# Performance work log

Hardware: AMD Instinct MI355X
Metric: run time of the kernel (lower is better)

The kernel has to match this reference:

```python
import jax, jax.numpy as jnp
import numpy as np

C = 192; H = 8; DH = C // H; FF = 384; SET = 36; NSET = 2048; N = NSET * SET
NBLK = 4; NLYR = 8
EPS = 1e-5
SCALE = np.float32(1.0 / np.sqrt(DH))


def _ln(x, w, b):
    m = jnp.mean(x, -1, keepdims=True)
    v = jnp.mean((x - m) ** 2, -1, keepdims=True)
    return (x - m) * jax.lax.rsqrt(v + EPS) * w + b


def _set_attn(src, pos, inds, mask, l, in_w, in_b, ow, ob, l1w, l1b, l2w, l2b, n1w, n1b, n2w, n2b):
    # gather voxel features into sets: [NSET, SET, C]
    feat = src[inds]
    q = feat + pos[inds]  # query == key == feat + pos_embed; value == feat
    qp = (q @ in_w[l, :C].T + in_b[l, :C]).reshape(NSET, SET, H, DH)
    kp = (q @ in_w[l, C:2 * C].T + in_b[l, C:2 * C]).reshape(NSET, SET, H, DH)
    vp = (feat @ in_w[l, 2 * C:].T + in_b[l, 2 * C:]).reshape(NSET, SET, H, DH)
    scores = jnp.einsum('sqhd,skhd->shqk', qp, kp) * SCALE
    scores = jnp.where(mask[:, None, None, :], jnp.float32(-1e9), scores)
    attn = jax.nn.softmax(scores, axis=-1)
    o = jnp.einsum('shqk,skhd->sqhd', attn, vp).reshape(NSET, SET, C)
    o = o @ ow[l].T + ob[l]
    # onnx_export scatter-back: placeholder[flatten_inds] = src2 (inds are a permutation)
    src2 = jnp.zeros_like(src).at[inds.reshape(-1)].set(o.reshape(-1, C))
    x = _ln(src + src2, n1w[l], n1b[l])
    ff = jax.nn.relu(x @ l1w[l].T + l1b[l]) @ l2w[l].T + l2b[l]
    return _ln(x + ff, n2w[l], n2b[l])


def _forward(feats, pos_embed, inds0, inds1, mask0, mask1, in_w, in_b, ow, ob,
             l1w, l1b, l2w, l2b, n1w, n1b, n2w, n2b, enw, enb, bnw, bnb):
    out = feats
    res = out
    for blk in range(NBLK):
        inds_t = inds0 if blk % 2 == 0 else inds1
        mask_t = mask0 if blk % 2 == 0 else mask1
        for s in range(2):
            l = 2 * blk + s
            ident = out
            x = _set_attn(out, pos_embed[blk, s], inds_t[s], mask_t[s], l,
                          in_w, in_b, ow, ob, l1w, l1b, l2w, l2b, n1w, n1b, n2w, n2b)
            out = _ln(x + ident, enw[l], enb[l])
        out = _ln(res + out, bnw[blk], bnb[blk])
        res = out
    return out


def setup_inputs() -> dict:
    key = jax.random.key(0)
    ks = jax.random.split(key, 16)
    s = jnp.float32(0.02)

    def perm(k):
        return jax.random.permutation(k, N).reshape(NSET, SET).astype(jnp.int32)

    inds0 = jnp.stack([perm(ks[1]), perm(ks[2])])
    inds1 = jnp.stack([perm(ks[3]), perm(ks[4])])
    mask0 = jnp.zeros((2, NSET, SET), dtype=bool)
    mask1 = jnp.zeros((2, NSET, SET), dtype=bool)
    return {
        'pillar_features': jax.random.normal(ks[0], (N, C), jnp.float32),
        'set_voxel_inds_tensor_shift_0': inds0,
        'set_voxel_inds_tensor_shift_1': inds1,
        'set_voxel_masks_tensor_shift_0': mask0,
        'set_voxel_masks_tensor_shift_1': mask1,
        'pos_embed_tensor': jax.random.normal(ks[5], (NBLK, 2, N, C), jnp.float32) * s,
        'in_proj_w': jax.random.normal(ks[6], (NLYR, 3 * C, C), jnp.float32) * s,
        'in_proj_b': jnp.zeros((NLYR, 3 * C), jnp.float32),
        'out_proj_w': jax.random.normal(ks[7], (NLYR, C, C), jnp.float32) * s,
        'out_proj_b': jnp.zeros((NLYR, C), jnp.float32),
        'lin1_w': jax.random.normal(ks[8], (NLYR, FF, C), jnp.float32) * s,
        'lin1_b': jnp.zeros((NLYR, FF), jnp.float32),
        'lin2_w': jax.random.normal(ks[9], (NLYR, C, FF), jnp.float32) * s,
        'lin2_b': jnp.zeros((NLYR, C), jnp.float32),
        'norm1_w': jnp.ones((NLYR, C), jnp.float32),
        'norm1_b': jnp.zeros((NLYR, C), jnp.float32),
        'norm2_w': jnp.ones((NLYR, C), jnp.float32),
        'norm2_b': jnp.zeros((NLYR, C), jnp.float32),
        'enc_norm_w': jnp.ones((NLYR, C), jnp.float32),
        'enc_norm_b': jnp.zeros((NLYR, C), jnp.float32),
        'blk_norm_w': jnp.ones((NBLK, C), jnp.float32),
        'blk_norm_b': jnp.zeros((NBLK, C), jnp.float32),
    }


def reference(pillar_features, set_voxel_inds_tensor_shift_0, set_voxel_inds_tensor_shift_1,
              set_voxel_masks_tensor_shift_0, set_voxel_masks_tensor_shift_1, pos_embed_tensor,
              in_proj_w, in_proj_b, out_proj_w, out_proj_b, lin1_w, lin1_b, lin2_w, lin2_b,
              norm1_w, norm1_b, norm2_w, norm2_b, enc_norm_w, enc_norm_b, blk_norm_w, blk_norm_b):
    return _forward(pillar_features, pos_embed_tensor,
                    set_voxel_inds_tensor_shift_0, set_voxel_inds_tensor_shift_1,
                    set_voxel_masks_tensor_shift_0, set_voxel_masks_tensor_shift_1,
                    in_proj_w, in_proj_b, out_proj_w, out_proj_b,
                    lin1_w, lin1_b, lin2_w, lin2_b,
                    norm1_w, norm1_b, norm2_w, norm2_b,
                    enc_norm_w, enc_norm_b, blk_norm_w, blk_norm_b)
```

## Files before the change

kernel.cpp:

```cpp
#include <hip/hip_runtime.h>
#include <stdint.h>


#define CC 192
#define FFD 384
#define NSETS 2048
#define SETSZ 36
#define NVOX (NSETS * SETSZ)
#define NCELEM ((size_t)NVOX * CC)
#define EPSV 1e-5f
#define SCALEV 0.2041241452319315f

typedef __bf16 bf16x8 __attribute__((ext_vector_type(8)));
typedef float f32x4 __attribute__((ext_vector_type(4)));

__device__ __forceinline__ float bflo(unsigned int u) {
  union { unsigned int i; float f; } v; v.i = u << 16; return v.f;
}
__device__ __forceinline__ float bfhi(unsigned int u) {
  union { unsigned int i; float f; } v; v.i = u & 0xffff0000u; return v.f;
}
__device__ __forceinline__ float bf2f(unsigned short s) {
  union { unsigned int i; float f; } v; v.i = ((unsigned int)s) << 16; return v.f;
}
__device__ __forceinline__ unsigned short f2bf(float f) {
  union { float f; unsigned int i; } v; v.f = f;
  return (unsigned short)((v.i + 0x7fffu + ((v.i >> 16) & 1u)) >> 16);
}
__device__ __forceinline__ unsigned int pack2(float a, float b) {
  return (unsigned int)f2bf(a) | ((unsigned int)f2bf(b) << 16);
}
__device__ __forceinline__ float wsum64(float v) {
#pragma unroll
  for (int off = 32; off > 0; off >>= 1) v += __shfl_xor(v, off, 64);
  return v;
}

__global__ __launch_bounds__(256) void cvt_xp(const float* __restrict__ pf,
                                              const float* __restrict__ pos,
                                              unsigned short* __restrict__ R,
                                              unsigned short* __restrict__ XP) {
  const size_t i = (size_t)blockIdx.x * 256 + threadIdx.x;
  const float4 a = ((const float4*)pf)[2 * i];
  const float4 b = ((const float4*)pf)[2 * i + 1];
  const float4 p = ((const float4*)pos)[2 * i];
  const float4 q = ((const float4*)pos)[2 * i + 1];
  uint4 r, x;
  r.x = pack2(a.x, a.y); r.y = pack2(a.z, a.w);
  r.z = pack2(b.x, b.y); r.w = pack2(b.z, b.w);
  x.x = pack2(a.x + p.x, a.y + p.y); x.y = pack2(a.z + p.z, a.w + p.w);
  x.z = pack2(b.x + q.x, b.y + q.y); x.w = pack2(b.z + q.z, b.w + q.w);
  ((uint4*)R)[i] = r;
  ((uint4*)XP)[i] = x;
}

__global__ __launch_bounds__(256) void cvt_wfrag(const float* __restrict__ src,
                                                 unsigned short* __restrict__ dst,
                                                 int N, int K, int total) {
  const int t = blockIdx.x * 256 + threadIdx.x;
  if (t >= total) return;
  const int lane = t & 63;
  const int f = t >> 6;
  const int nks = K >> 5;
  const int ks = f % nks;
  const int rem = f / nks;
  const int nnt = N >> 4;
  const int nt = rem % nnt;
  const int l = rem / nnt;
  const int row = nt * 16 + (lane & 15);
  const int k0 = ks * 32 + (lane >> 4) * 8;
  const float* s = src + ((size_t)l * N + row) * K + k0;
  const float4 a = *(const float4*)s;
  const float4 b = *(const float4*)(s + 4);
  uint4 o;
  o.x = pack2(a.x, a.y); o.y = pack2(a.z, a.w);
  o.z = pack2(b.x, b.y); o.w = pack2(b.z, b.w);
  *(uint4*)(dst + (size_t)t * 8) = o;
}

__global__ __launch_bounds__(256, 2) void qkvattn_kernel(
    const unsigned short* __restrict__ XP, const unsigned short* __restrict__ Xv,
    const int* __restrict__ inds, const unsigned short* __restrict__ Wf,
    const float* __restrict__ bias, unsigned short* __restrict__ Oset) {
  __shared__ __align__(16) unsigned short sQ[36 * 200];
  __shared__ __align__(16) unsigned short sK[36 * 200];
  __shared__ __align__(16) unsigned short sVt[192 * 72];
  __shared__ __align__(16) unsigned short sP[4 * 36 * 72];
  const int set = blockIdx.x, tid = threadIdx.x;
  const int lane = tid & 63, wid = tid >> 6;
  const int l15 = lane & 15, l4 = lane >> 4;

  int rowg[3];
#pragma unroll
  for (int mt = 0; mt < 3; ++mt) {
    const int rr = mt * 16 + l15;
    rowg[mt] = inds[set * SETSZ + (rr < 36 ? rr : 35)];
  }
  for (int c = tid; c < 1344; c += 256) {
    const int d = c / 7, j = c - d * 7;
    *(uint2*)(sVt + d * 72 + 36 + j * 4) = make_uint2(0, 0);
  }
  for (int c = lane; c < 72; c += 64) {
    *(uint4*)(sP + wid * 2592 + (c >> 1) * 72 + 48 + (c & 1) * 8) = make_uint4(0, 0, 0, 0);
  }

  f32x4 acc[9][3] = {};
#pragma unroll
  for (int ks = 0; ks < 6; ++ks) {
    const int k0 = ks * 32 + l4 * 8;
    bf16x8 aP[3], aV[3];
#pragma unroll
    for (int mt = 0; mt < 3; ++mt) {
      aP[mt] = *(const bf16x8*)(XP + (size_t)rowg[mt] * CC + k0);
      aV[mt] = *(const bf16x8*)(Xv + (size_t)rowg[mt] * CC + k0);
    }
#pragma unroll
    for (int i = 0; i < 9; ++i) {
      const int nt = wid + 4 * i;
      const bf16x8 bw = *(const bf16x8*)(Wf + (((size_t)nt * 6 + ks) * 64 + lane) * 8);
      const bool isV = (nt >= 24);
#pragma unroll
      for (int mt = 0; mt < 3; ++mt)
        acc[i][mt] = __builtin_amdgcn_mfma_f32_16x16x32_bf16(
            isV ? aV[mt] : aP[mt], bw, acc[i][mt], 0, 0, 0);
    }
  }
#pragma unroll
  for (int i = 0; i < 9; ++i) {
    const int nt = wid + 4 * i;
    const int b = nt / 12;
    const int col = nt * 16 - b * CC + l15;
    const float bv = bias[nt * 16 + l15];
    if (b < 2) {
      unsigned short* d = (b == 0) ? sQ : sK;
#pragma unroll
      for (int mt = 0; mt < 3; ++mt)
#pragma unroll
        for (int j = 0; j < 4; ++j) {
          const int r = mt * 16 + l4 * 4 + j;
          if (r < 36) d[r * 200 + col] = f2bf(acc[i][mt][j] + bv);
        }
    } else {
#pragma unroll
      for (int mt = 0; mt < 3; ++mt)
#pragma unroll
        for (int j = 0; j < 4; ++j)
          sVt[col * 72 + mt * 16 + l4 * 4 + j] = f2bf(acc[i][mt][j] + bv);
    }
  }
  __syncthreads();

  const bf16x8 zed = {};
  const f32x4 fz = {};
  f32x4 oout[2][3][2];
#pragma unroll
  for (int hh = 0; hh < 2; ++hh) {
    const int h = wid + 4 * hh;
    const int hb = h * 24;
    bf16x8 aq[3], bk[3];
#pragma unroll
    for (int t = 0; t < 3; ++t) {
      const int rq0 = t * 16 + l15;
      const int rq = rq0 < 36 ? rq0 : 35;
      const bf16x8 qv = *(const bf16x8*)(sQ + rq * 200 + hb + l4 * 8);
      const bf16x8 kv = *(const bf16x8*)(sK + rq * 200 + hb + l4 * 8);
      aq[t] = (l4 == 3) ? zed : qv;
      bk[t] = (l4 == 3) ? zed : kv;
    }
    f32x4 sc[3][3];
#pragma unroll
    for (int mt = 0; mt < 3; ++mt)
#pragma unroll
      for (int nt = 0; nt < 3; ++nt)
        sc[mt][nt] = __builtin_amdgcn_mfma_f32_16x16x32_bf16(aq[mt], bk[nt], fz, 0, 0, 0);
#pragma unroll
    for (int mt = 0; mt < 3; ++mt)
#pragma unroll
      for (int j = 0; j < 4; ++j) {
        const int r = mt * 16 + l4 * 4 + j;
        const float v0 = sc[mt][0][j] * SCALEV;
        const float v1 = sc[mt][1][j] * SCALEV;
        const float v2 = (l15 >= 4) ? -1e30f : sc[mt][2][j] * SCALEV;
        float mx = fmaxf(fmaxf(v0, v1), v2);
#pragma unroll
        for (int off = 1; off < 16; off <<= 1) mx = fmaxf(mx, __shfl_xor(mx, off, 64));
        const float p0 = __expf(v0 - mx), p1 = __expf(v1 - mx), p2 = __expf(v2 - mx);
        float sm = p0 + p1 + p2;
#pragma unroll
        for (int off = 1; off < 16; off <<= 1) sm += __shfl_xor(sm, off, 64);
        const float inv = 1.f / sm;
        if (r < 36) {
          sP[wid * 2592 + r * 72 + l15] = f2bf(p0 * inv);
          sP[wid * 2592 + r * 72 + 16 + l15] = f2bf(p1 * inv);
          sP[wid * 2592 + r * 72 + 32 + l15] = f2bf(p2 * inv);
        }
      }
    f32x4 oa[3][2] = {};
#pragma unroll
    for (int ks2 = 0; ks2 < 2; ++ks2) {
      bf16x8 bvv[2];
#pragma unroll
      for (int nt16 = 0; nt16 < 2; ++nt16) {
        const int dd0 = hb + nt16 * 16 + l15;
        const int dd = dd0 < 192 ? dd0 : 191;
        bvv[nt16] = *(const bf16x8*)(sVt + dd * 72 + ks2 * 32 + l4 * 8);
      }
#pragma unroll
      for (int mt = 0; mt < 3; ++mt) {
        const int rp0 = mt * 16 + l15;
        const int rp = rp0 < 36 ? rp0 : 35;
        const bf16x8 ap = *(const bf16x8*)(sP + wid * 2592 + rp * 72 + ks2 * 32 + l4 * 8);
#pragma unroll
        for (int nt16 = 0; nt16 < 2; ++nt16)
          oa[mt][nt16] = __builtin_amdgcn_mfma_f32_16x16x32_bf16(ap, bvv[nt16], oa[mt][nt16], 0, 0, 0);
      }
    }
#pragma unroll
    for (int mt = 0; mt < 3; ++mt)
#pragma unroll
      for (int nt16 = 0; nt16 < 2; ++nt16)
        oout[hh][mt][nt16] = oa[mt][nt16];
  }
  __syncthreads();
  unsigned short* const sO = sP;
#pragma unroll
  for (int hh = 0; hh < 2; ++hh) {
    const int hb = (wid + 4 * hh) * 24;
#pragma unroll
    for (int mt = 0; mt < 3; ++mt)
#pragma unroll
      for (int j = 0; j < 4; ++j) {
        const int r = mt * 16 + l4 * 4 + j;
        if (r < 36) {
          sO[r * 200 + hb + l15] = f2bf(oout[hh][mt][0][j]);
          if (l15 < 8) sO[r * 200 + hb + 16 + l15] = f2bf(oout[hh][mt][1][j]);
        }
      }
  }
  __syncthreads();
  unsigned short* dst = Oset + (size_t)set * SETSZ * CC;
  for (int c = tid; c < 864; c += 256) {
    const int r = c / 24, cl = c - r * 24;
    *(uint4*)(dst + (size_t)r * CC + cl * 8) = *(const uint4*)(sO + r * 200 + cl * 8);
  }
}

#define PBM 16
__global__ __launch_bounds__(256, 4) void post_kernel(
    const unsigned short* __restrict__ Oset, const int* __restrict__ inds,
    const unsigned short* __restrict__ src,
    unsigned short* __restrict__ Xout, unsigned short* __restrict__ Rbuf,
    const unsigned short* __restrict__ Wo, const float* __restrict__ bo,
    const unsigned short* __restrict__ W1, const float* __restrict__ b1,
    const unsigned short* __restrict__ W2, const float* __restrict__ b2,
    const float* __restrict__ n1w, const float* __restrict__ n1b,
    const float* __restrict__ n2w, const float* __restrict__ n2b,
    const float* __restrict__ enw, const float* __restrict__ enb,
    const float* __restrict__ bnw, const float* __restrict__ bnb,
    const float* __restrict__ posn, unsigned short* __restrict__ XPout,
    float* __restrict__ fout) {
  __shared__ __align__(16) unsigned char smem[36864];
  __shared__ int sGi[PBM];
  unsigned short* const sO = (unsigned short*)smem;
  unsigned short* const sXb = (unsigned short*)(smem + 6144);
  float* const sX = (float*)(smem + 12288);
  unsigned short* const sH = (unsigned short*)(smem + 24576);
  float* const sY = (float*)smem;

  const int tid = threadIdx.x;
  const int m0 = blockIdx.x * PBM;
  const int lane = tid & 63, wid = tid >> 6;
  const int l15 = lane & 15, l4 = lane >> 4;

  if (tid < PBM) sGi[tid] = inds[m0 + tid];
  for (int c = tid; c < 384; c += 256) {
    const int row = c / 24, cl = c - row * 24;
    const int cs = cl ^ (row & 7);
    *(uint4*)(sO + row * CC + cl * 8) = *(const uint4*)(Oset + (size_t)(m0 + row) * CC + cs * 8);
  }
  __syncthreads();

  f32x4 acc1[3] = {};
#pragma unroll
  for (int ks = 0; ks < 6; ++ks) {
    const int kb = ks * 4 + l4;
    const bf16x8 a = *(const bf16x8*)(sO + l15 * CC + ((kb ^ (l15 & 7)) << 3));
#pragma unroll
    for (int ni = 0; ni < 3; ++ni) {
      const bf16x8 bw = *(const bf16x8*)(Wo + (((size_t)(wid * 3 + ni) * 6 + ks) * 64 + lane) * 8);
      acc1[ni] = __builtin_amdgcn_mfma_f32_16x16x32_bf16(a, bw, acc1[ni], 0, 0, 0);
    }
  }
#pragma unroll
  for (int ni = 0; ni < 3; ++ni) {
    const int col = wid * 48 + ni * 16 + l15;
    const float bv = bo[col];
#pragma unroll
    for (int j = 0; j < 4; ++j) {
      const int row = l4 * 4 + j;
      sX[row * CC + col] = acc1[ni][j] + bv + bf2f(src[(size_t)sGi[row] * CC + col]);
    }
  }
  __syncthreads();

#pragma unroll
  for (int k = 0; k < 4; ++k) {
    const int r = wid * 4 + k;
    const int sh = (r & 7) << 3;
    const float v0 = sX[r * CC + lane], v1 = sX[r * CC + lane + 64], v2 = sX[r * CC + lane + 128];
    const float mn = wsum64(v0 + v1 + v2) * (1.f / CC);
    const float d0 = v0 - mn, d1 = v1 - mn, d2 = v2 - mn;
    const float rs = rsqrtf(wsum64(d0 * d0 + d1 * d1 + d2 * d2) * (1.f / CC) + EPSV);
#pragma unroll
    for (int i = 0; i < 3; ++i) {
      const int c = lane + 64 * i;
      const float x = (sX[r * CC + c] - mn) * rs * n1w[c] + n1b[c];
      sX[r * CC + c] = x;
      sXb[r * CC + (c ^ sh)] = f2bf(x);
    }
  }
  __syncthreads();

  f32x4 acc2[6] = {};
#pragma unroll
  for (int ks = 0; ks < 6; ++ks) {
    const int kb = ks * 4 + l4;
    const bf16x8 a = *(const bf16x8*)(sXb + l15 * CC + ((kb ^ (l15 & 7)) << 3));
#pragma unroll
    for (int i = 0; i < 6; ++i) {
      const int nt = wid + 4 * i;
      const bf16x8 bw = *(const bf16x8*)(W1 + (((size_t)nt * 6 + ks) * 64 + lane) * 8);
      acc2[i] = __builtin_amdgcn_mfma_f32_16x16x32_bf16(a, bw, acc2[i], 0, 0, 0);
    }
  }
#pragma unroll
  for (int i = 0; i < 6; ++i) {
    const int nt = wid + 4 * i;
    const int col = nt * 16 + l15;
    const float bv = b1[col];
#pragma unroll
    for (int j = 0; j < 4; ++j) {
      const int row = l4 * 4 + j;
      sH[row * FFD + (col ^ ((row & 7) << 3))] = f2bf(fmaxf(acc2[i][j] + bv, 0.f));
    }
  }
  __syncthreads();

  f32x4 acc3[3] = {};
#pragma unroll
  for (int ks = 0; ks < 12; ++ks) {
    const int kb = ks * 4 + l4;
    const bf16x8 a = *(const bf16x8*)(sH + l15 * FFD + ((kb ^ (l15 & 7)) << 3));
#pragma unroll
    for (int i = 0; i < 3; ++i) {
      const int nt = wid + 4 * i;
      const bf16x8 bw = *(const bf16x8*)(W2 + (((size_t)nt * 12 + ks) * 64 + lane) * 8);
      acc3[i] = __builtin_amdgcn_mfma_f32_16x16x32_bf16(a, bw, acc3[i], 0, 0, 0);
    }
  }
#pragma unroll
  for (int i = 0; i < 3; ++i) {
    const int nt = wid + 4 * i;
    const int col = nt * 16 + l15;
    const float bv = b2[col];
#pragma unroll
    for (int j = 0; j < 4; ++j) {
      const int row = l4 * 4 + j;
      sY[row * CC + col] = acc3[i][j] + bv + sX[row * CC + col];
    }
  }
  __syncthreads();

#pragma unroll
  for (int k = 0; k < 4; ++k) {
    const int r = wid * 4 + k;
    const size_t g = (size_t)sGi[r] * CC;
    const float v0 = sY[r * CC + lane], v1 = sY[r * CC + lane + 64], v2 = sY[r * CC + lane + 128];
    float mn = wsum64(v0 + v1 + v2) * (1.f / CC);
    float d0 = v0 - mn, d1 = v1 - mn, d2 = v2 - mn;
    float rs = rsqrtf(wsum64(d0 * d0 + d1 * d1 + d2 * d2) * (1.f / CC) + EPSV);
    float t0 = (v0 - mn) * rs * n2w[lane] + n2b[lane] + bf2f(src[g + lane]);
    float t1 = (v1 - mn) * rs * n2w[lane + 64] + n2b[lane + 64] + bf2f(src[g + lane + 64]);
    float t2 = (v2 - mn) * rs * n2w[lane + 128] + n2b[lane + 128] + bf2f(src[g + lane + 128]);
    mn = wsum64(t0 + t1 + t2) * (1.f / CC);
    d0 = t0 - mn; d1 = t1 - mn; d2 = t2 - mn;
    rs = rsqrtf(wsum64(d0 * d0 + d1 * d1 + d2 * d2) * (1.f / CC) + EPSV);
    float o0 = d0 * rs * enw[lane] + enb[lane];
    float o1 = d1 * rs * enw[lane + 64] + enb[lane + 64];
    float o2 = d2 * rs * enw[lane + 128] + enb[lane + 128];
    if (Rbuf) {
      o0 += bf2f(Rbuf[g + lane]);
      o1 += bf2f(Rbuf[g + lane + 64]);
      o2 += bf2f(Rbuf[g + lane + 128]);
      mn = wsum64(o0 + o1 + o2) * (1.f / CC);
      d0 = o0 - mn; d1 = o1 - mn; d2 = o2 - mn;
      rs = rsqrtf(wsum64(d0 * d0 + d1 * d1 + d2 * d2) * (1.f / CC) + EPSV);
      o0 = d0 * rs * bnw[lane] + bnb[lane];
      o1 = d1 * rs * bnw[lane + 64] + bnb[lane + 64];
      o2 = d2 * rs * bnw[lane + 128] + bnb[lane + 128];
      Rbuf[g + lane] = f2bf(o0);
      Rbuf[g + lane + 64] = f2bf(o1);
      Rbuf[g + lane + 128] = f2bf(o2);
      if (fout) {
        fout[g + lane] = o0;
        fout[g + lane + 64] = o1;
        fout[g + lane + 128] = o2;
      }
    } else {
      Xout[g + lane] = f2bf(o0);
      Xout[g + lane + 64] = f2bf(o1);
      Xout[g + lane + 128] = f2bf(o2);
    }
    if (XPout) {
      XPout[g + lane] = f2bf(o0 + posn[g + lane]);
      XPout[g + lane + 64] = f2bf(o1 + posn[g + lane + 64]);
      XPout[g + lane + 128] = f2bf(o2 + posn[g + lane + 128]);
    }
  }
}

extern "C" void kernel_launch(void* const* d_in, const int* in_sizes, int n_in,
                              void* d_out, int out_size, void* d_ws, size_t ws_size,
                              hipStream_t stream) {
  const float* pf  = (const float*)d_in[0];
  const int* inds0 = (const int*)d_in[1];
  const int* inds1 = (const int*)d_in[2];
  const float* pos = (const float*)d_in[5];
  const float* in_w = (const float*)d_in[6];
  const float* in_b = (const float*)d_in[7];
  const float* ow = (const float*)d_in[8];
  const float* ob = (const float*)d_in[9];
  const float* l1w = (const float*)d_in[10];
  const float* l1b = (const float*)d_in[11];
  const float* l2w = (const float*)d_in[12];
  const float* l2b = (const float*)d_in[13];
  const float* n1w = (const float*)d_in[14];
  const float* n1b = (const float*)d_in[15];
  const float* n2w = (const float*)d_in[16];
  const float* n2b = (const float*)d_in[17];
  const float* enw = (const float*)d_in[18];
  const float* enb = (const float*)d_in[19];
  const float* bnw = (const float*)d_in[20];
  const float* bnb = (const float*)d_in[21];

  unsigned short* X0   = (unsigned short*)d_ws;
  unsigned short* R    = X0 + NCELEM;
  unsigned short* XPb  = R + NCELEM;
  unsigned short* Oset = XPb + NCELEM;
  const size_t WQL = (size_t)36 * 6 * 64 * 8;
  const size_t WOL = (size_t)12 * 6 * 64 * 8;
  const size_t W1L = (size_t)24 * 6 * 64 * 8;
  const size_t W2L = (size_t)12 * 12 * 64 * 8;
  unsigned short* Wq  = Oset + NCELEM;
  unsigned short* Wo  = Wq + 8 * WQL;
  unsigned short* W1f = Wo + 8 * WOL;
  unsigned short* W2f = W1f + 8 * W1L;
  unsigned short* XPa = (unsigned short*)d_out;
  (void)ws_size;

  cvt_xp<<<6912, 256, 0, stream>>>(pf, pos, R, XPa);
  cvt_wfrag<<<(int)(8 * WQL / 8 / 256), 256, 0, stream>>>(in_w, Wq, 576, 192, (int)(8 * WQL / 8));
  cvt_wfrag<<<(int)(8 * WOL / 8 / 256), 256, 0, stream>>>(ow, Wo, 192, 192, (int)(8 * WOL / 8));
  cvt_wfrag<<<(int)(8 * W1L / 8 / 256), 256, 0, stream>>>(l1w, W1f, 384, 192, (int)(8 * W1L / 8));
  cvt_wfrag<<<(int)(8 * W2L / 8 / 256), 256, 0, stream>>>(l2w, W2f, 192, 384, (int)(8 * W2L / 8));

  const unsigned short* cur = R;
  for (int blk = 0; blk < 4; ++blk) {
    const int* indsb = (blk % 2 == 0) ? inds0 : inds1;
    for (int s = 0; s < 2; ++s) {
      const int l = 2 * blk + s;
      const int* ind = indsb + (size_t)s * NVOX;
      const unsigned short* XPi = (l & 1) ? XPb : XPa;
      unsigned short* XPo = (l == 7) ? nullptr : ((l & 1) ? XPa : XPb);
      const float* posn = (l == 7) ? nullptr : pos + (size_t)(l + 1) * NCELEM;
      qkvattn_kernel<<<NSETS, 256, 0, stream>>>(
          XPi, cur, ind, Wq + (size_t)l * WQL, in_b + (size_t)l * 576, Oset);
      post_kernel<<<NVOX / PBM, 256, 0, stream>>>(
          Oset, ind, cur,
          (s == 0) ? X0 : nullptr,
          (s == 1) ? R : nullptr,
          Wo + (size_t)l * WOL, ob + (size_t)l * CC,
          W1f + (size_t)l * W1L, l1b + (size_t)l * FFD,
          W2f + (size_t)l * W2L, l2b + (size_t)l * CC,
          n1w + (size_t)l * CC, n1b + (size_t)l * CC,
          n2w + (size_t)l * CC, n2b + (size_t)l * CC,
          enw + (size_t)l * CC, enb + (size_t)l * CC,
          (s == 1) ? bnw + (size_t)blk * CC : nullptr,
          (s == 1) ? bnb + (size_t)blk * CC : nullptr,
          posn, XPo,
          (l == 7) ? (float*)d_out : nullptr);
      cur = (s == 0) ? X0 : R;
    }
  }
}
```

Before: 1.659 ms.

## Fuse attention and post-processing into a single per-set layer kernel

Merges the QKV/attention kernel and the out-projection/FFN/LayerNorm kernel into one kernel per set, so the attention output stays in shared memory instead of round-tripping through a global Oset buffer. The post stage now works on 36 rows per block (3 M-tiles padded to 48) rather than 16-row blocks, and shared memory is reused across phases. This removes one launch per layer and the global write and read of the attention output. In exchange, LDS use rises to about 77 KB per block, which can limit occupancy, and the padded M-tiles waste some MFMA work.

```diff
diff --git a/kernel.cpp b/kernel.cpp
--- a/kernel.cpp
+++ b/kernel.cpp
@@ -78,18 +78,38 @@
   *(uint4*)(dst + (size_t)t * 8) = o;
 }
 
-__global__ __launch_bounds__(256, 2) void qkvattn_kernel(
+__global__ __launch_bounds__(256, 2) void layer_kernel(
     const unsigned short* __restrict__ XP, const unsigned short* __restrict__ Xv,
-    const int* __restrict__ inds, const unsigned short* __restrict__ Wf,
-    const float* __restrict__ bias, unsigned short* __restrict__ Oset) {
-  __shared__ __align__(16) unsigned short sQ[36 * 200];
-  __shared__ __align__(16) unsigned short sK[36 * 200];
-  __shared__ __align__(16) unsigned short sVt[192 * 72];
-  __shared__ __align__(16) unsigned short sP[4 * 36 * 72];
+    const int* __restrict__ inds,
+    const unsigned short* __restrict__ Wq, const float* __restrict__ qb,
+    const unsigned short* __restrict__ Wo, const float* __restrict__ bo,
+    const unsigned short* __restrict__ W1, const float* __restrict__ b1,
+    const unsigned short* __restrict__ W2, const float* __restrict__ b2,
+    const float* __restrict__ n1w, const float* __restrict__ n1b,
+    const float* __restrict__ n2w, const float* __restrict__ n2b,
+    const float* __restrict__ enw, const float* __restrict__ enb,
+    const float* __restrict__ bnw, const float* __restrict__ bnb,
+    unsigned short* __restrict__ Xout, unsigned short* __restrict__ Rbuf,
+    const float* __restrict__ posn, unsigned short* __restrict__ XPout,
+    float* __restrict__ fout) {
+  __shared__ __align__(16) unsigned char smem[77184];
+  __shared__ int gi[SETSZ];
+  unsigned short* const sVt = (unsigned short*)smem;
+  unsigned short* const sQ  = (unsigned short*)(smem + 27648);
+  unsigned short* const sK  = (unsigned short*)(smem + 42048);
+  unsigned short* const sP  = (unsigned short*)(smem + 56448);
+  float* const sXf = (float*)smem;
+  unsigned short* const sXb = (unsigned short*)(smem + 27648);
+  unsigned short* const sH  = (unsigned short*)(smem + 42048);
+  unsigned short* const sO  = (unsigned short*)(smem + 56448);
+  float* const sY = (float*)(smem + 42048);
+
   const int set = blockIdx.x, tid = threadIdx.x;
   const int lane = tid & 63, wid = tid >> 6;
   const int l15 = lane & 15, l4 = lane >> 4;
 
+  if (tid < SETSZ) gi[tid] = inds[set * SETSZ + tid];
+
   int rowg[3];
 #pragma unroll
   for (int mt = 0; mt < 3; ++mt) {
@@ -104,48 +124,50 @@
     *(uint4*)(sP + wid * 2592 + (c >> 1) * 72 + 48 + (c & 1) * 8) = make_uint4(0, 0, 0, 0);
   }
 
-  f32x4 acc[9][3] = {};
-#pragma unroll
-  for (int ks = 0; ks < 6; ++ks) {
-    const int k0 = ks * 32 + l4 * 8;
-    bf16x8 aP[3], aV[3];
-#pragma unroll
-    for (int mt = 0; mt < 3; ++mt) {
-      aP[mt] = *(const bf16x8*)(XP + (size_t)rowg[mt] * CC + k0);
-      aV[mt] = *(const bf16x8*)(Xv + (size_t)rowg[mt] * CC + k0);
+  {
+    f32x4 acc[9][3] = {};
+#pragma unroll
+    for (int ks = 0; ks < 6; ++ks) {
+      const int k0 = ks * 32 + l4 * 8;
+      bf16x8 aP[3], aV[3];
+#pragma unroll
+      for (int mt = 0; mt < 3; ++mt) {
+        aP[mt] = *(const bf16x8*)(XP + (size_t)rowg[mt] * CC + k0);
+        aV[mt] = *(const bf16x8*)(Xv + (size_t)rowg[mt] * CC + k0);
+      }
+#pragma unroll
+      for (int i = 0; i < 9; ++i) {
+        const int nt = wid + 4 * i;
+        const bf16x8 bw = *(const bf16x8*)(Wq + (((size_t)nt * 6 + ks) * 64 + lane) * 8);
+        const bool isV = (nt >= 24);
+#pragma unroll
+        for (int mt = 0; mt < 3; ++mt)
+          acc[i][mt] = __builtin_amdgcn_mfma_f32_16x16x32_bf16(
+              isV ? aV[mt] : aP[mt], bw, acc[i][mt], 0, 0, 0);
+      }
     }
 #pragma unroll
     for (int i = 0; i < 9; ++i) {
       const int nt = wid + 4 * i;
-      const bf16x8 bw = *(const bf16x8*)(Wf + (((size_t)nt * 6 + ks) * 64 + lane) * 8);
-      const bool isV = (nt >= 24);
-#pragma unroll
-      for (int mt = 0; mt < 3; ++mt)
-        acc[i][mt] = __builtin_amdgcn_mfma_f32_16x16x32_bf16(
-            isV ? aV[mt] : aP[mt], bw, acc[i][mt], 0, 0, 0);
-    }
-  }
-#pragma unroll
-  for (int i = 0; i < 9; ++i) {
-    const int nt = wid + 4 * i;
-    const int b = nt / 12;
-    const int col = nt * 16 - b * CC + l15;
-    const float bv = bias[nt * 16 + l15];
-    if (b < 2) {
-      unsigned short* d = (b == 0) ? sQ : sK;
-#pragma unroll
-      for (int mt = 0; mt < 3; ++mt)
-#pragma unroll
-        for (int j = 0; j < 4; ++j) {
-          const int r = mt * 16 + l4 * 4 + j;
-          if (r < 36) d[r * 200 + col] = f2bf(acc[i][mt][j] + bv);
-        }
-    } else {
-#pragma unroll
-      for (int mt = 0; mt < 3; ++mt)
-#pragma unroll
-        for (int j = 0; j < 4; ++j)
-          sVt[col * 72 + mt * 16 + l4 * 4 + j] = f2bf(acc[i][mt][j] + bv);
+      const int b = nt / 12;
+      const int col = nt * 16 - b * CC + l15;
+      const float bv = qb[nt * 16 + l15];
+      if (b < 2) {
+        unsigned short* d = (b == 0) ? sQ : sK;
+#pragma unroll
+        for (int mt = 0; mt < 3; ++mt)
+#pragma unroll
+          for (int j = 0; j < 4; ++j) {
+            const int r = mt * 16 + l4 * 4 + j;
+            if (r < 36) d[r * 200 + col] = f2bf(acc[i][mt][j] + bv);
+          }
+      } else {
+#pragma unroll
+        for (int mt = 0; mt < 3; ++mt)
+#pragma unroll
+          for (int j = 0; j < 4; ++j)
+            sVt[col * 72 + mt * 16 + l4 * 4 + j] = f2bf(acc[i][mt][j] + bv);
+      }
     }
   }
   __syncthreads();
@@ -222,7 +244,6 @@
         oout[hh][mt][nt16] = oa[mt][nt16];
   }
   __syncthreads();
-  unsigned short* const sO = sP;
 #pragma unroll
   for (int hh = 0; hh < 2; ++hh) {
     const int hb = (wid + 4 * hh) * 24;
@@ -238,150 +259,145 @@
       }
   }
   __syncthreads();
-  unsigned short* dst = Oset + (size_t)set * SETSZ * CC;
-  for (int c = tid; c < 864; c += 256) {
-    const int r = c / 24, cl = c - r * 24;
-    *(uint4*)(dst + (size_t)r * CC + cl * 8) = *(const uint4*)(sO + r * 200 + cl * 8);
-  }
-}
-
-#define PBM 16
-__global__ __launch_bounds__(256, 4) void post_kernel(
-    const unsigned short* __restrict__ Oset, const int* __restrict__ inds,
-    const unsigned short* __restrict__ src,
-    unsigned short* __restrict__ Xout, unsigned short* __restrict__ Rbuf,
-    const unsigned short* __restrict__ Wo, const float* __restrict__ bo,
-    const unsigned short* __restrict__ W1, const float* __restrict__ b1,
-    const unsigned short* __restrict__ W2, const float* __restrict__ b2,
-    const float* __restrict__ n1w, const float* __restrict__ n1b,
-    const float* __restrict__ n2w, const float* __restrict__ n2b,
-    const float* __restrict__ enw, const float* __restrict__ enb,
-    const float* __restrict__ bnw, const float* __restrict__ bnb,
-    const float* __restrict__ posn, unsigned short* __restrict__ XPout,
-    float* __restrict__ fout) {
-  __shared__ __align__(16) unsigned char smem[36864];
-  __shared__ int sGi[PBM];
-  unsigned short* const sO = (unsigned short*)smem;
-  unsigned short* const sXb = (unsigned short*)(smem + 6144);
-  float* const sX = (float*)(smem + 12288);
-  unsigned short* const sH = (unsigned short*)(smem + 24576);
-  float* const sY = (float*)smem;
-
-  const int tid = threadIdx.x;
-  const int m0 = blockIdx.x * PBM;
-  const int lane = tid & 63, wid = tid >> 6;
-  const int l15 = lane & 15, l4 = lane >> 4;
-
-  if (tid < PBM) sGi[tid] = inds[m0 + tid];
-  for (int c = tid; c < 384; c += 256) {
-    const int row = c / 24, cl = c - row * 24;
-    const int cs = cl ^ (row & 7);
-    *(uint4*)(sO + row * CC + cl * 8) = *(const uint4*)(Oset + (size_t)(m0 + row) * CC + cs * 8);
-  }
-  __syncthreads();
-
-  f32x4 acc1[3] = {};
-#pragma unroll
-  for (int ks = 0; ks < 6; ++ks) {
-    const int kb = ks * 4 + l4;
-    const bf16x8 a = *(const bf16x8*)(sO + l15 * CC + ((kb ^ (l15 & 7)) << 3));
+
+  {
+    f32x4 acc1[3][3] = {};
+#pragma unroll
+    for (int ks = 0; ks < 6; ++ks) {
+      bf16x8 a[3];
+#pragma unroll
+      for (int mt = 0; mt < 3; ++mt) {
+        const int row = mt * 16 + l15;
+        const int rc = row < 36 ? row : 35;
+        a[mt] = *(const bf16x8*)(sO + rc * 200 + (ks * 4 + l4) * 8);
+      }
+#pragma unroll
+      for (int ni = 0; ni < 3; ++ni) {
+        const bf16x8 bw = *(const bf16x8*)(Wo + (((size_t)(wid * 3 + ni) * 6 + ks) * 64 + lane) * 8);
+#pragma unroll
+        for (int mt = 0; mt < 3; ++mt)
+          acc1[ni][mt] = __builtin_amdgcn_mfma_f32_16x16x32_bf16(a[mt], bw, acc1[ni][mt], 0, 0, 0);
+      }
+    }
 #pragma unroll
     for (int ni = 0; ni < 3; ++ni) {
-      const bf16x8 bw = *(const bf16x8*)(Wo + (((size_t)(wid * 3 + ni) * 6 + ks) * 64 + lane) * 8);
-      acc1[ni] = __builtin_amdgcn_mfma_f32_16x16x32_bf16(a, bw, acc1[ni], 0, 0, 0);
-    }
-  }
-#pragma unroll
-  for (int ni = 0; ni < 3; ++ni) {
-    const int col = wid * 48 + ni * 16 + l15;
-    const float bv = bo[col];
-#pragma unroll
-    for (int j = 0; j < 4; ++j) {
-      const int row = l4 * 4 + j;
-      sX[row * CC + col] = acc1[ni][j] + bv + bf2f(src[(size_t)sGi[row] * CC + col]);
-    }
-  }
-  __syncthreads();
-
-#pragma unroll
-  for (int k = 0; k < 4; ++k) {
-    const int r = wid * 4 + k;
+      const int col = wid * 48 + ni * 16 + l15;
+      const float bv = bo[col];
+#pragma unroll
+      for (int mt = 0; mt < 3; ++mt)
+#pragma unroll
+        for (int j = 0; j < 4; ++j) {
+          const int row = mt * 16 + l4 * 4 + j;
+          if (row < 36)
+            sXf[row * CC + col] = acc1[ni][mt][j] + bv + bf2f(Xv[(size_t)gi[row] * CC + col]);
+        }
+    }
+  }
+  __syncthreads();
+
+  for (int r = wid; r < 36; r += 4) {
     const int sh = (r & 7) << 3;
-    const float v0 = sX[r * CC + lane], v1 = sX[r * CC + lane + 64], v2 = sX[r * CC + lane + 128];
+    const float v0 = sXf[r * CC + lane], v1 = sXf[r * CC + lane + 64], v2 = sXf[r * CC + lane + 128];
     const float mn = wsum64(v0 + v1 + v2) * (1.f / CC);
     const float d0 = v0 - mn, d1 = v1 - mn, d2 = v2 - mn;
     const float rs = rsqrtf(wsum64(d0 * d0 + d1 * d1 + d2 * d2) * (1.f / CC) + EPSV);
 #pragma unroll
     for (int i = 0; i < 3; ++i) {
       const int c = lane + 64 * i;
-      const float x = (sX[r * CC + c] - mn) * rs * n1w[c] + n1b[c];
-      sX[r * CC + c] = x;
+      const float x = (sXf[r * CC + c] - mn) * rs * n1w[c] + n1b[c];
+      sXf[r * CC + c] = x;
       sXb[r * CC + (c ^ sh)] = f2bf(x);
     }
   }
   __syncthreads();
 
-  f32x4 acc2[6] = {};
-#pragma unroll
-  for (int ks = 0; ks < 6; ++ks) {
-    const int kb = ks * 4 + l4;
-    const bf16x8 a = *(const bf16x8*)(sXb + l15 * CC + ((kb ^ (l15 & 7)) << 3));
+  {
+    f32x4 acc2[6][3] = {};
+#pragma unroll
+    for (int ks = 0; ks < 6; ++ks) {
+      const int kb = ks * 4 + l4;
+      bf16x8 a[3];
+#pragma unroll
+      for (int mt = 0; mt < 3; ++mt) {
+        const int row = mt * 16 + l15;
+        const int rc = row < 36 ? row : 35;
+        a[mt] = *(const bf16x8*)(sXb + rc * CC + ((kb ^ (rc & 7)) << 3));
+      }
+#pragma unroll
+      for (int i = 0; i < 6; ++i) {
+        const int nt = wid + 4 * i;
+        const bf16x8 bw = *(const bf16x8*)(W1 + (((size_t)nt * 6 + ks) * 64 + lane) * 8);
+#pragma unroll
+        for (int mt = 0; mt < 3; ++mt)
+          acc2[i][mt] = __builtin_amdgcn_mfma_f32_16x16x32_bf16(a[mt], bw, acc2[i][mt], 0, 0, 0);
+      }
+    }
+    __syncthreads();
 #pragma unroll
     for (int i = 0; i < 6; ++i) {
       const int nt = wid + 4 * i;
-      const bf16x8 bw = *(const bf16x8*)(W1 + (((size_t)nt * 6 + ks) * 64 + lane) * 8);
-      acc2[i] = __builtin_amdgcn_mfma_f32_16x16x32_bf16(a, bw, acc2[i], 0, 0, 0);
-    }
-  }
-#pragma unroll
-  for (int i = 0; i < 6; ++i) {
-    const int nt = wid + 4 * i;
-    const int col = nt * 16 + l15;
-    const float bv = b1[col];
-#pragma unroll
-    for (int j = 0; j < 4; ++j) {
-      const int row = l4 * 4 + j;
-      sH[row * FFD + (col ^ ((row & 7) << 3))] = f2bf(fmaxf(acc2[i][j] + bv, 0.f));
-    }
-  }
-  __syncthreads();
-
-  f32x4 acc3[3] = {};
-#pragma unroll
-  for (int ks = 0; ks < 12; ++ks) {
-    const int kb = ks * 4 + l4;
-    const bf16x8 a = *(const bf16x8*)(sH + l15 * FFD + ((kb ^ (l15 & 7)) << 3));
+      const int col = nt * 16 + l15;
+      const float bv = b1[col];
+#pragma unroll
+      for (int mt = 0; mt < 3; ++mt)
+#pragma unroll
+        for (int j = 0; j < 4; ++j) {
+          const int row = mt * 16 + l4 * 4 + j;
+          if (row < 36)
+            sH[row * FFD + (col ^ ((row & 7) << 3))] = f2bf(fmaxf(acc2[i][mt][j] + bv, 0.f));
+        }
+    }
+  }
+  __syncthreads();
+
+  {
+    f32x4 acc3[3][3] = {};
+#pragma unroll
+    for (int ks = 0; ks < 12; ++ks) {
+      const int kb = ks * 4 + l4;
+      bf16x8 a[3];
+#pragma unroll
+      for (int mt = 0; mt < 3; ++mt) {
+        const int row = mt * 16 + l15;
+        const int rc = row < 36 ? row : 35;
+        a[mt] = *(const bf16x8*)(sH + rc * FFD + ((kb ^ (rc & 7)) << 3));
+      }
+#pragma unroll
+      for (int i = 0; i < 3; ++i) {
+        const int nt = wid + 4 * i;
+        const bf16x8 bw = *(const bf16x8*)(W2 + (((size_t)nt * 12 + ks) * 64 + lane) * 8);
+#pragma unroll
+        for (int mt = 0; mt < 3; ++mt)
+          acc3[i][mt] = __builtin_amdgcn_mfma_f32_16x16x32_bf16(a[mt], bw, acc3[i][mt], 0, 0, 0);
+      }
+    }
+    __syncthreads();
 #pragma unroll
     for (int i = 0; i < 3; ++i) {
       const int nt = wid + 4 * i;
-      const bf16x8 bw = *(const bf16x8*)(W2 + (((size_t)nt * 12 + ks) * 64 + lane) * 8);
-      acc3[i] = __builtin_amdgcn_mfma_f32_16x16x32_bf16(a, bw, acc3[i], 0, 0, 0);
-    }
-  }
-#pragma unroll
-  for (int i = 0; i < 3; ++i) {
-    const int nt = wid + 4 * i;
-    const int col = nt * 16 + l15;
-    const float bv = b2[col];
-#pragma unroll
-    for (int j = 0; j < 4; ++j) {
-      const int row = l4 * 4 + j;
-      sY[row * CC + col] = acc3[i][j] + bv + sX[row * CC + col];
-    }
-  }
-  __syncthreads();
-
-#pragma unroll
-  for (int k = 0; k < 4; ++k) {
-    const int r = wid * 4 + k;
-    const size_t g = (size_t)sGi[r] * CC;
+      const int col = nt * 16 + l15;
+      const float bv = b2[col];
+#pragma unroll
+      for (int mt = 0; mt < 3; ++mt)
+#pragma unroll
+        for (int j = 0; j < 4; ++j) {
+          const int row = mt * 16 + l4 * 4 + j;
+          if (row < 36)
+            sY[row * CC + col] = acc3[i][mt][j] + bv + sXf[row * CC + col];
+        }
+    }
+  }
+  __syncthreads();
+
+  for (int r = wid; r < 36; r += 4) {
+    const size_t g = (size_t)gi[r] * CC;
     const float v0 = sY[r * CC + lane], v1 = sY[r * CC + lane + 64], v2 = sY[r * CC + lane + 128];
     float mn = wsum64(v0 + v1 + v2) * (1.f / CC);
     float d0 = v0 - mn, d1 = v1 - mn, d2 = v2 - mn;
     float rs = rsqrtf(wsum64(d0 * d0 + d1 * d1 + d2 * d2) * (1.f / CC) + EPSV);
-    float t0 = (v0 - mn) * rs * n2w[lane] + n2b[lane] + bf2f(src[g + lane]);
-    float t1 = (v1 - mn) * rs * n2w[lane + 64] + n2b[lane + 64] + bf2f(src[g + lane + 64]);
-    float t2 = (v2 - mn) * rs * n2w[lane + 128] + n2b[lane + 128] + bf2f(src[g + lane + 128]);
+    float t0 = (v0 - mn) * rs * n2w[lane] + n2b[lane] + bf2f(Xv[g + lane]);
+    float t1 = (v1 - mn) * rs * n2w[lane + 64] + n2b[lane + 64] + bf2f(Xv[g + lane + 64]);
+    float t2 = (v2 - mn) * rs * n2w[lane + 128] + n2b[lane + 128] + bf2f(Xv[g + lane + 128]);
     mn = wsum64(t0 + t1 + t2) * (1.f / CC);
     d0 = t0 - mn; d1 = t1 - mn; d2 = t2 - mn;
     rs = rsqrtf(wsum64(d0 * d0 + d1 * d1 + d2 * d2) * (1.f / CC) + EPSV);
@@ -443,15 +459,14 @@
   const float* bnw = (const float*)d_in[20];
   const float* bnb = (const float*)d_in[21];
 
-  unsigned short* X0   = (unsigned short*)d_ws;
-  unsigned short* R    = X0 + NCELEM;
-  unsigned short* XPb  = R + NCELEM;
-  unsigned short* Oset = XPb + NCELEM;
+  unsigned short* X0  = (unsigned short*)d_ws;
+  unsigned short* R   = X0 + NCELEM;
+  unsigned short* XPb = R + NCELEM;
   const size_t WQL = (size_t)36 * 6 * 64 * 8;
   const size_t WOL = (size_t)12 * 6 * 64 * 8;
   const size_t W1L = (size_t)24 * 6 * 64 * 8;
   const size_t W2L = (size_t)12 * 12 * 64 * 8;
-  unsigned short* Wq  = Oset + NCELEM;
+  unsigned short* Wq  = XPb + NCELEM;
   unsigned short* Wo  = Wq + 8 * WQL;
   unsigned short* W1f = Wo + 8 * WOL;
   unsigned short* W2f = W1f + 8 * W1L;
@@ -473,12 +488,9 @@
       const unsigned short* XPi = (l & 1) ? XPb : XPa;
       unsigned short* XPo = (l == 7) ? nullptr : ((l & 1) ? XPa : XPb);
       const float* posn = (l == 7) ? nullptr : pos + (size_t)(l + 1) * NCELEM;
-      qkvattn_kernel<<<NSETS, 256, 0, stream>>>(
-          XPi, cur, ind, Wq + (size_t)l * WQL, in_b + (size_t)l * 576, Oset);
-      post_kernel<<<NVOX / PBM, 256, 0, stream>>>(
-          Oset, ind, cur,
-          (s == 0) ? X0 : nullptr,
-          (s == 1) ? R : nullptr,
+      layer_kernel<<<NSETS, 256, 0, stream>>>(
+          XPi, cur, ind,
+          Wq + (size_t)l * WQL, in_b + (size_t)l * 576,
           Wo + (size_t)l * WOL, ob + (size_t)l * CC,
           W1f + (size_t)l * W1L, l1b + (size_t)l * FFD,
           W2f + (size_t)l * W2L, l2b + (size_t)l * CC,
@@ -487,6 +499,8 @@
           enw + (size_t)l * CC, enb + (size_t)l * CC,
           (s == 1) ? bnw + (size_t)blk * CC : nullptr,
           (s == 1) ? bnb + (size_t)blk * CC : nullptr,
+          (s == 0) ? X0 : nullptr,
+          (s == 1) ? R : nullptr,
           posn, XPo,
           (l == 7) ? (float*)d_out : nullptr);
       cur = (s == 0) ? X0 : R;
```

After: 1.950 ms. 1.18x slower.

## Shrink LDS footprint in attention and post kernels to raise occupancy

Applied to the files above, without the earlier changes.

The attention kernel now uses unpadded, XOR-swizzled Q/K tiles and 36-wide V/P tiles instead of padded 200/72-wide ones. The 36-wide key dimension is handled as one full 32-wide MFMA step plus a zero-padded tail step, which removes the zero-fill loops. Per-head outputs go straight to global memory instead of through a staging buffer with two block barriers. The post kernel aliases its LDS regions more tightly, at the cost of an extra barrier, and both kernels get higher launch-bound occupancy hints. The tradeoff is narrower, uncoalesced 2-byte global stores and possible register pressure under the tighter launch bounds.

```diff
diff --git a/kernel.cpp b/kernel.cpp
--- a/kernel.cpp
+++ b/kernel.cpp
@@ -34,6 +34,15 @@
 #pragma unroll
   for (int off = 32; off > 0; off >>= 1) v += __shfl_xor(v, off, 64);
   return v;
+}
+__device__ __forceinline__ bf16x8 ld44(const unsigned short* p) {
+  const uint2 lo = *(const uint2*)p;
+  const uint2 hi = *(const uint2*)(p + 4);
+  union { uint4 u; bf16x8 v; } c; c.u = make_uint4(lo.x, lo.y, hi.x, hi.y); return c.v;
+}
+__device__ __forceinline__ bf16x8 ld4z(const unsigned short* p) {
+  const uint2 lo = *(const uint2*)p;
+  union { uint4 u; bf16x8 v; } c; c.u = make_uint4(lo.x, lo.y, 0u, 0u); return c.v;
 }
 
 __global__ __launch_bounds__(256) void cvt_xp(const float* __restrict__ pf,
@@ -78,14 +87,14 @@
   *(uint4*)(dst + (size_t)t * 8) = o;
 }
 
-__global__ __launch_bounds__(256, 2) void qkvattn_kernel(
+__global__ __launch_bounds__(256, 3) void qkvattn_kernel(
     const unsigned short* __restrict__ XP, const unsigned short* __restrict__ Xv,
     const int* __restrict__ inds, const unsigned short* __restrict__ Wf,
     const float* __restrict__ bias, unsigned short* __restrict__ Oset) {
-  __shared__ __align__(16) unsigned short sQ[36 * 200];
-  __shared__ __align__(16) unsigned short sK[36 * 200];
-  __shared__ __align__(16) unsigned short sVt[192 * 72];
-  __shared__ __align__(16) unsigned short sP[4 * 36 * 72];
+  __shared__ __align__(16) unsigned short sQ[36 * 192];
+  __shared__ __align__(16) unsigned short sK[36 * 192];
+  __shared__ __align__(16) unsigned short sVt[192 * 36];
+  __shared__ __align__(16) unsigned short sP[4 * 36 * 36];
   const int set = blockIdx.x, tid = threadIdx.x;
   const int lane = tid & 63, wid = tid >> 6;
   const int l15 = lane & 15, l4 = lane >> 4;
@@ -95,13 +104,6 @@
   for (int mt = 0; mt < 3; ++mt) {
     const int rr = mt * 16 + l15;
     rowg[mt] = inds[set * SETSZ + (rr < 36 ? rr : 35)];
-  }
-  for (int c = tid; c < 1344; c += 256) {
-    const int d = c / 7, j = c - d * 7;
-    *(uint2*)(sVt + d * 72 + 36 + j * 4) = make_uint2(0, 0);
-  }
-  for (int c = lane; c < 72; c += 64) {
-    *(uint4*)(sP + wid * 2592 + (c >> 1) * 72 + 48 + (c & 1) * 8) = make_uint4(0, 0, 0, 0);
   }
 
   f32x4 acc[9][3] = {};
@@ -133,26 +135,30 @@
     const float bv = bias[nt * 16 + l15];
     if (b < 2) {
       unsigned short* d = (b == 0) ? sQ : sK;
+      const int c8 = col >> 3, c7 = col & 7;
 #pragma unroll
       for (int mt = 0; mt < 3; ++mt)
 #pragma unroll
         for (int j = 0; j < 4; ++j) {
           const int r = mt * 16 + l4 * 4 + j;
-          if (r < 36) d[r * 200 + col] = f2bf(acc[i][mt][j] + bv);
+          if (r < 36) d[r * 192 + ((c8 ^ (r & 7)) << 3) + c7] = f2bf(acc[i][mt][j] + bv);
         }
     } else {
 #pragma unroll
       for (int mt = 0; mt < 3; ++mt)
 #pragma unroll
-        for (int j = 0; j < 4; ++j)
-          sVt[col * 72 + mt * 16 + l4 * 4 + j] = f2bf(acc[i][mt][j] + bv);
+        for (int j = 0; j < 4; ++j) {
+          const int r = mt * 16 + l4 * 4 + j;
+          if (r < 36) sVt[col * 36 + r] = f2bf(acc[i][mt][j] + bv);
+        }
     }
   }
   __syncthreads();
 
   const bf16x8 zed = {};
   const f32x4 fz = {};
-  f32x4 oout[2][3][2];
+  unsigned short* const sPw = sP + wid * (36 * 36);
+  unsigned short* const odst = Oset + (size_t)set * SETSZ * CC;
 #pragma unroll
   for (int hh = 0; hh < 2; ++hh) {
     const int h = wid + 4 * hh;
@@ -162,8 +168,9 @@
     for (int t = 0; t < 3; ++t) {
       const int rq0 = t * 16 + l15;
       const int rq = rq0 < 36 ? rq0 : 35;
-      const bf16x8 qv = *(const bf16x8*)(sQ + rq * 200 + hb + l4 * 8);
-      const bf16x8 kv = *(const bf16x8*)(sK + rq * 200 + hb + l4 * 8);
+      const int cs = ((3 * h + l4) ^ (rq & 7)) << 3;
+      const bf16x8 qv = *(const bf16x8*)(sQ + rq * 192 + cs);
+      const bf16x8 kv = *(const bf16x8*)(sK + rq * 192 + cs);
       aq[t] = (l4 == 3) ? zed : qv;
       bk[t] = (l4 == 3) ? zed : kv;
     }
@@ -190,63 +197,63 @@
         for (int off = 1; off < 16; off <<= 1) sm += __shfl_xor(sm, off, 64);
         const float inv = 1.f / sm;
         if (r < 36) {
-          sP[wid * 2592 + r * 72 + l15] = f2bf(p0 * inv);
-          sP[wid * 2592 + r * 72 + 16 + l15] = f2bf(p1 * inv);
-          sP[wid * 2592 + r * 72 + 32 + l15] = f2bf(p2 * inv);
+          sPw[r * 36 + l15] = f2bf(p0 * inv);
+          sPw[r * 36 + 16 + l15] = f2bf(p1 * inv);
+          if (l15 < 4) sPw[r * 36 + 32 + l15] = f2bf(p2 * inv);
         }
       }
     f32x4 oa[3][2] = {};
-#pragma unroll
-    for (int ks2 = 0; ks2 < 2; ++ks2) {
+    {
       bf16x8 bvv[2];
 #pragma unroll
       for (int nt16 = 0; nt16 < 2; ++nt16) {
         const int dd0 = hb + nt16 * 16 + l15;
         const int dd = dd0 < 192 ? dd0 : 191;
-        bvv[nt16] = *(const bf16x8*)(sVt + dd * 72 + ks2 * 32 + l4 * 8);
+        bvv[nt16] = ld44(sVt + dd * 36 + l4 * 8);
       }
 #pragma unroll
       for (int mt = 0; mt < 3; ++mt) {
         const int rp0 = mt * 16 + l15;
         const int rp = rp0 < 36 ? rp0 : 35;
-        const bf16x8 ap = *(const bf16x8*)(sP + wid * 2592 + rp * 72 + ks2 * 32 + l4 * 8);
-#pragma unroll
-        for (int nt16 = 0; nt16 < 2; ++nt16)
-          oa[mt][nt16] = __builtin_amdgcn_mfma_f32_16x16x32_bf16(ap, bvv[nt16], oa[mt][nt16], 0, 0, 0);
+        const bf16x8 ap = ld44(sPw + rp * 36 + l4 * 8);
+        oa[mt][0] = __builtin_amdgcn_mfma_f32_16x16x32_bf16(ap, bvv[0], oa[mt][0], 0, 0, 0);
+        oa[mt][1] = __builtin_amdgcn_mfma_f32_16x16x32_bf16(ap, bvv[1], oa[mt][1], 0, 0, 0);
       }
     }
-#pragma unroll
-    for (int mt = 0; mt < 3; ++mt)
-#pragma unroll
-      for (int nt16 = 0; nt16 < 2; ++nt16)
-        oout[hh][mt][nt16] = oa[mt][nt16];
-  }
-  __syncthreads();
-  unsigned short* const sO = sP;
-#pragma unroll
-  for (int hh = 0; hh < 2; ++hh) {
-    const int hb = (wid + 4 * hh) * 24;
+    {
+      bf16x8 bvv[2];
+      if (l4 == 0) {
+#pragma unroll
+        for (int nt16 = 0; nt16 < 2; ++nt16) {
+          const int dd0 = hb + nt16 * 16 + l15;
+          const int dd = dd0 < 192 ? dd0 : 191;
+          bvv[nt16] = ld4z(sVt + dd * 36 + 32);
+        }
+      } else { bvv[0] = zed; bvv[1] = zed; }
+#pragma unroll
+      for (int mt = 0; mt < 3; ++mt) {
+        const int rp0 = mt * 16 + l15;
+        const int rp = rp0 < 36 ? rp0 : 35;
+        const bf16x8 ap = (l4 == 0) ? ld4z(sPw + rp * 36 + 32) : zed;
+        oa[mt][0] = __builtin_amdgcn_mfma_f32_16x16x32_bf16(ap, bvv[0], oa[mt][0], 0, 0, 0);
+        oa[mt][1] = __builtin_amdgcn_mfma_f32_16x16x32_bf16(ap, bvv[1], oa[mt][1], 0, 0, 0);
+      }
+    }
 #pragma unroll
     for (int mt = 0; mt < 3; ++mt)
 #pragma unroll
       for (int j = 0; j < 4; ++j) {
         const int r = mt * 16 + l4 * 4 + j;
         if (r < 36) {
-          sO[r * 200 + hb + l15] = f2bf(oout[hh][mt][0][j]);
-          if (l15 < 8) sO[r * 200 + hb + 16 + l15] = f2bf(oout[hh][mt][1][j]);
+          odst[(size_t)r * CC + hb + l15] = f2bf(oa[mt][0][j]);
+          if (l15 < 8) odst[(size_t)r * CC + hb + 16 + l15] = f2bf(oa[mt][1][j]);
         }
       }
   }
-  __syncthreads();
-  unsigned short* dst = Oset + (size_t)set * SETSZ * CC;
-  for (int c = tid; c < 864; c += 256) {
-    const int r = c / 24, cl = c - r * 24;
-    *(uint4*)(dst + (size_t)r * CC + cl * 8) = *(const uint4*)(sO + r * 200 + cl * 8);
-  }
 }
 
 #define PBM 16
-__global__ __launch_bounds__(256, 4) void post_kernel(
+__global__ __launch_bounds__(256, 5) void post_kernel(
     const unsigned short* __restrict__ Oset, const int* __restrict__ inds,
     const unsigned short* __restrict__ src,
     unsigned short* __restrict__ Xout, unsigned short* __restrict__ Rbuf,
@@ -259,13 +266,13 @@
     const float* __restrict__ bnw, const float* __restrict__ bnb,
     const float* __restrict__ posn, unsigned short* __restrict__ XPout,
     float* __restrict__ fout) {
-  __shared__ __align__(16) unsigned char smem[36864];
+  __shared__ __align__(16) unsigned char smem[30720];
   __shared__ int sGi[PBM];
   unsigned short* const sO = (unsigned short*)smem;
-  unsigned short* const sXb = (unsigned short*)(smem + 6144);
-  float* const sX = (float*)(smem + 12288);
-  unsigned short* const sH = (unsigned short*)(smem + 24576);
-  float* const sY = (float*)smem;
+  unsigned short* const sXb = (unsigned short*)smem;
+  float* const sX = (float*)(smem + 6144);
+  unsigned short* const sH = (unsigned short*)(smem + 18432);
+  float* const sY = (float*)(smem + 18432);
 
   const int tid = threadIdx.x;
   const int m0 = blockIdx.x * PBM;
@@ -358,6 +365,7 @@
       acc3[i] = __builtin_amdgcn_mfma_f32_16x16x32_bf16(a, bw, acc3[i], 0, 0, 0);
     }
   }
+  __syncthreads();
 #pragma unroll
   for (int i = 0; i < 3; ++i) {
     const int nt = wid + 4 * i;
```

Result: slower. 2.083 ms (+25.5%).
